# Performance work log

Hardware: AMD Instinct MI355X
Metric: run time of the kernel (lower is better)

## Reference

```python
import jax, jax.numpy as jnp
import numpy as np

D_MODEL = 1024
N_HEADS = 16
D_K = 64  # per-head dim and the scaling denominator used by the module
NEG = -1e9  # stand-in for -inf in masked_fill (rows are never fully masked)


def setup_inputs() -> dict:
    key = jax.random.key(0)
    ks = jax.random.split(key, 8)
    B, M, N = 2, 2048, 2048
    q = jax.random.normal(ks[0], (B, M, D_MODEL), dtype=jnp.float32)
    k = jax.random.normal(ks[1], (B, N, D_MODEL), dtype=jnp.float32)
    v = jax.random.normal(ks[2], (B, N, D_MODEL), dtype=jnp.float32)
    mask = jax.random.randint(ks[3], (B, M, N), 0, 2).astype(jnp.bool_)
    # xavier_uniform for square [d,d] weights: limit = sqrt(6/(d+d))
    lim = float(np.sqrt(6.0 / (D_MODEL + D_MODEL)))
    Wq = jax.random.uniform(ks[4], (D_MODEL, D_MODEL), jnp.float32, -lim, lim)
    Wk = jax.random.uniform(ks[5], (D_MODEL, D_MODEL), jnp.float32, -lim, lim)
    Wv = jax.random.uniform(ks[6], (D_MODEL, D_MODEL), jnp.float32, -lim, lim)
    Wo = jax.random.uniform(ks[7], (D_MODEL, D_MODEL), jnp.float32, -lim, lim)
    return {"q": q, "k": k, "v": v, "mask": mask,
            "Wq": Wq, "Wk": Wk, "Wv": Wv, "Wo": Wo}


def _split_heads(x):
    # (B, S, D) -> (B, H, S, Dh); the torch split/cat-on-batch trick is
    # mathematically identical to this standard head reshape.
    B, S, _ = x.shape
    return x.reshape(B, S, N_HEADS, D_K).transpose(0, 2, 1, 3)


def reference(q, k, v, mask, Wq, Wk, Wv, Wo):
    qw = _split_heads(q @ Wq.T)  # (B,H,M,Dh)
    kw = _split_heads(k @ Wk.T)  # (B,H,N,Dh)
    vw = _split_heads(v @ Wv.T)  # (B,H,N,Dh)
    scores = jnp.einsum('bhmd,bhnd->bhmn', qw, kw)
    scores = jnp.where(mask[:, None, :, :], NEG, scores)
    attn = jax.nn.softmax(scores / jnp.sqrt(jnp.float32(D_K)), axis=-1)
    ctx = jnp.einsum('bhmn,bhnd->bhmd', attn, vw)
    B, _, M, _ = ctx.shape
    ctx = ctx.transpose(0, 2, 1, 3).reshape(B, M, D_MODEL)
    return ctx @ Wo.T
```

## Files before the change

kernel.cpp:

```cpp
#include <hip/hip_runtime.h>
#include <hip/hip_bf16.h>
#include <stdint.h>
#include <string.h>

#define SEQ   2048
#define DM    1024
#define NH    16
#define NB    2

typedef __attribute__((ext_vector_type(8))) short bf16x8;
typedef __attribute__((ext_vector_type(4))) float f32x4;
typedef unsigned short u16;
typedef unsigned int   u32;

__device__ __forceinline__ u16 f2bf(float f) {
    u32 u = __float_as_uint(f);
    u += 0x7FFF + ((u >> 16) & 1);
    return (u16)(u >> 16);
}
__device__ __forceinline__ u32 pk2bf(float a, float b) {
    __hip_bfloat162 p = __float22bfloat162_rn(make_float2(a, b));
    u32 u; memcpy(&u, &p, 4); return u;
}
__device__ __forceinline__ float fexp2(float x) {
#if __has_builtin(__builtin_amdgcn_exp2f)
    return __builtin_amdgcn_exp2f(x);
#else
    return exp2f(x);
#endif
}
__device__ __forceinline__ void gl_lds16(const void* g, void* l) {
    __builtin_amdgcn_global_load_lds(
        (const __attribute__((address_space(1))) u32*)g,
        (__attribute__((address_space(3))) u32*)l, 16, 0, 0);
}

struct CvtArgs {
    const float* s[7];
    u16* d[7];
    float scale[7];
    int start[8];
};
__global__ __launch_bounds__(256) void cvt_kernel(CvtArgs a) {
    int bid = blockIdx.x;
    int seg = 0;
#pragma unroll
    for (int i = 1; i < 7; ++i) if (bid >= a.start[i]) seg = i;
    float sc = a.scale[seg];
    size_t base = (size_t)(bid - a.start[seg]) * 2048 + threadIdx.x * 8;
    const float4* s4 = (const float4*)(a.s[seg] + base);
    float4 x = s4[0], y = s4[1];
    u32 r[4];
    r[0] = pk2bf(x.x*sc, x.y*sc); r[1] = pk2bf(x.z*sc, x.w*sc);
    r[2] = pk2bf(y.x*sc, y.y*sc); r[3] = pk2bf(y.z*sc, y.w*sc);
    *(uint4*)(a.d[seg] + base) = *(uint4*)r;
}

__global__ void maskpack_kernel(const int* __restrict__ mask,
                                unsigned int* __restrict__ bits) {
    int gid = blockIdx.x * 256 + threadIdx.x;
    int m = mask[gid];
    unsigned long long bal = __ballot(m != 0);
    int lane = threadIdx.x & 63;
    if (lane == 0)       bits[gid >> 5] = (u32)(bal & 0xFFFFFFFFull);
    else if (lane == 32) bits[gid >> 5] = (u32)(bal >> 32);
}

template<int RT>
__device__ __forceinline__ void gemm_body(const u16* __restrict__ A,
                                          const u16* __restrict__ Bm,
                                          void* __restrict__ Y,
                                          int rtile, int ctile, int mode,
                                          u16* sA, u16* sB) {
    constexpr int ABUF = RT * 32 * 32;
    constexpr int BBUF = 128 * 32;
    const int tid  = threadIdx.x;
    const int wv   = tid >> 6, lane = tid & 63;
    const int quad = lane >> 4, ln = lane & 15;
    const int wr   = wv >> 1,  wc  = wv & 1;

    const int lr4 = lane >> 2;
    const int lcc = ((lane & 3) ^ ((lane >> 3) & 3)) * 8;

    const u16* gA[RT/2]; u16* lA[RT/2];
#pragma unroll
    for (int s = 0; s < RT/2; ++s) {
        int seg = wv * (RT/2) + s;
        gA[s] = A + (size_t)(rtile * (RT*32) + seg*16 + lr4) * 1024 + lcc;
        lA[s] = sA + seg * 512;
    }
    const u16* gB[2]; u16* lB[2];
#pragma unroll
    for (int s = 0; s < 2; ++s) {
        int seg = wv * 2 + s;
        gB[s] = Bm + (size_t)(ctile * 128 + seg*16 + lr4) * 1024 + lcc;
        lB[s] = sB + seg * 512;
    }

    f32x4 acc[RT][4];
#pragma unroll
    for (int i = 0; i < RT; ++i)
#pragma unroll
        for (int j = 0; j < 4; ++j) acc[i][j] = (f32x4){0.f,0.f,0.f,0.f};

    const int c0 = (quad ^ ((ln >> 1) & 3)) * 8;

#pragma unroll
    for (int s = 0; s < RT/2; ++s) gl_lds16(gA[s], lA[s]);
#pragma unroll
    for (int s = 0; s < 2; ++s)    gl_lds16(gB[s], lB[s]);

    for (int kt = 0; kt < 32; ++kt) {
        __syncthreads();
        if (kt < 31) {
            int nb = (kt + 1) & 1;
#pragma unroll
            for (int s = 0; s < RT/2; ++s)
                gl_lds16(gA[s] + (kt+1)*32, lA[s] + nb*ABUF);
#pragma unroll
            for (int s = 0; s < 2; ++s)
                gl_lds16(gB[s] + (kt+1)*32, lB[s] + nb*BBUF);
        }
        const u16* sAb = sA + (kt & 1) * ABUF;
        const u16* sBb = sB + (kt & 1) * BBUF;
        bf16x8 af[RT], bfr[4];
#pragma unroll
        for (int rt = 0; rt < RT; ++rt)
            af[rt] = *(const bf16x8*)(sAb + (wr*(RT*16) + rt*16 + ln) * 32 + c0);
#pragma unroll
        for (int ct = 0; ct < 4; ++ct)
            bfr[ct] = *(const bf16x8*)(sBb + (wc*64 + ct*16 + ln) * 32 + c0);
#pragma unroll
        for (int rt = 0; rt < RT; ++rt)
#pragma unroll
            for (int ct = 0; ct < 4; ++ct)
                acc[rt][ct] = __builtin_amdgcn_mfma_f32_16x16x32_bf16(
                    af[rt], bfr[ct], acc[rt][ct], 0, 0, 0);
    }

#pragma unroll
    for (int rt = 0; rt < RT; ++rt) {
#pragma unroll
        for (int ct = 0; ct < 4; ++ct) {
#pragma unroll
            for (int i = 0; i < 4; ++i) {
                int R = rtile*(RT*32) + wr*(RT*16) + rt*16 + quad*4 + i;
                int C = ctile*128 + wc*64 + ct*16 + ln;
                float val = acc[rt][ct][i];
                if (mode == 0) {
                    int b = R >> 11, s = R & 2047, h = C >> 6, d = C & 63;
                    ((u16*)Y)[((size_t)((b*NH + h) * SEQ + s) << 6) + d] = f2bf(val);
                } else if (mode == 1) {
                    int h = R >> 6, d = R & 63, b = C >> 11, n = C & 2047;
                    ((u16*)Y)[((size_t)((b*NH + h) * 64 + d) << 11) + n] = f2bf(val);
                } else {
                    ((float*)Y)[(size_t)R * 1024 + C] = val;
                }
            }
        }
    }
}

struct QKVArgs { const u16* A[3]; const u16* B[3]; u16* Y[3]; };

__global__ __launch_bounds__(256) void gemm_qkv(QKVArgs g) {
    __shared__ u16 sA[2 * 128 * 32];
    __shared__ u16 sB[2 * 128 * 32];
    int z = blockIdx.z;
    if (z == 2)
        gemm_body<4>(g.A[2], g.B[2], g.Y[2], blockIdx.y, blockIdx.x, 1, sA, sB);
    else
        gemm_body<4>(g.A[z], g.B[z], g.Y[z], blockIdx.x, blockIdx.y, 0, sA, sB);
}

__global__ __launch_bounds__(256) void gemm_out(const u16* __restrict__ A,
                                                const u16* __restrict__ Bm,
                                                float* __restrict__ Y) {
    __shared__ u16 sA[2 * 64 * 32];
    __shared__ u16 sB[2 * 128 * 32];
    gemm_body<2>(A, Bm, Y, blockIdx.x, blockIdx.y, 2, sA, sB);
}

__global__ __launch_bounds__(256) void attn_kernel(
    const u16* __restrict__ qw,
    const u16* __restrict__ kw,
    const u16* __restrict__ vt,
    const u32* __restrict__ mbits,
    u16* __restrict__ ctx) {

    constexpr int PST = 68;
    __shared__ u16 sK[2 * 64 * 64];
    __shared__ u16 sV[2 * 64 * 64];
    __shared__ u16 sP[4 * 32 * PST];

    const int mtile = blockIdx.x;
    const int bh    = blockIdx.y;
    const int b     = bh >> 4;
    const int tid   = threadIdx.x;
    const int wv    = tid >> 6, lane = tid & 63;
    const int quad  = lane >> 4, ln = lane & 15;
    const int m0    = mtile * 128;

    const size_t hbase = (size_t)bh * SEQ * 64;

    bf16x8 qf[2][2];
#pragma unroll
    for (int mt = 0; mt < 2; ++mt) {
        const u16* qp = qw + hbase + (size_t)(m0 + (wv*2+mt)*16 + ln) * 64 + quad*8;
        qf[mt][0] = *(const bf16x8*)(qp);
        qf[mt][1] = *(const bf16x8*)(qp + 32);
    }

    f32x4 o[2][4], lsum[2];
#pragma unroll
    for (int mt = 0; mt < 2; ++mt) {
        lsum[mt] = (f32x4){0.f,0.f,0.f,0.f};
#pragma unroll
        for (int j = 0; j < 4; ++j) o[mt][j] = (f32x4){0.f,0.f,0.f,0.f};
    }

    bf16x8 ones;
#pragma unroll
    for (int i = 0; i < 8; ++i) ones[i] = (short)0x3F80;

    const u32* mbase = mbits + (size_t)(b * SEQ + m0 + wv*32 + quad*4) * 64;
    const u32 mlo = 1u << ln;
    const u32 mhi = 1u << (ln + 16);

    const int lr = lane >> 3;
    const int lc = (lane & 7) ^ lr;
    const u16* gK[2]; const u16* gV[2];
    u16 *lK[2], *lV[2];
#pragma unroll
    for (int s = 0; s < 2; ++s) {
        int seg = s * 4 + wv;
        gK[s] = kw + hbase + (size_t)(seg*8 + lr) * 64 + lc*8;
        gV[s] = vt + hbase + (size_t)(seg*8 + lr) * SEQ + lc*8;
        lK[s] = sK + seg * 512;
        lV[s] = sV + seg * 512;
    }

    const int c0 = (quad ^ (ln & 7)) * 8;
    u16* sPw = sP + wv * 32 * PST;

#pragma unroll
    for (int s = 0; s < 2; ++s) { gl_lds16(gK[s], lK[s]); gl_lds16(gV[s], lV[s]); }
    uint2 wwA[2][4];
#pragma unroll
    for (int mt = 0; mt < 2; ++mt)
#pragma unroll
        for (int i = 0; i < 4; ++i)
            wwA[mt][i] = *(const uint2*)(mbase + (mt*16 + i)*64);

    for (int nt = 0; nt < SEQ / 64; ++nt) {
        __syncthreads();
        uint2 wwB[2][4];
        if (nt < SEQ/64 - 1) {
            int nb = (nt + 1) & 1;
#pragma unroll
            for (int s = 0; s < 2; ++s) {
                gl_lds16(gK[s] + (size_t)(nt+1) * 4096, lK[s] + nb*4096);
                gl_lds16(gV[s] + (nt+1) * 64,           lV[s] + nb*4096);
            }
#pragma unroll
            for (int mt = 0; mt < 2; ++mt)
#pragma unroll
                for (int i = 0; i < 4; ++i)
                    wwB[mt][i] = *(const uint2*)(mbase + (mt*16 + i)*64 + (nt+1)*2);
        }
        const u16* sKb = sK + (nt & 1) * 4096;
        const u16* sVb = sV + (nt & 1) * 4096;

        f32x4 s4[2][4];
#pragma unroll
        for (int ct = 0; ct < 4; ++ct) {
            const u16* kp = sKb + (ct*16 + ln) * 64;
            bf16x8 k0 = *(const bf16x8*)(kp + c0);
            bf16x8 k1 = *(const bf16x8*)(kp + (c0 ^ 32));
#pragma unroll
            for (int mt = 0; mt < 2; ++mt) {
                f32x4 z = (f32x4){0.f, 0.f, 0.f, 0.f};
                z = __builtin_amdgcn_mfma_f32_16x16x32_bf16(qf[mt][0], k0, z, 0, 0, 0);
                z = __builtin_amdgcn_mfma_f32_16x16x32_bf16(qf[mt][1], k1, z, 0, 0, 0);
                s4[mt][ct] = z;
            }
        }

#pragma unroll
        for (int mt = 0; mt < 2; ++mt) {
#pragma unroll
            for (int ct = 0; ct < 4; ++ct) {
                const u32 mb = (ct & 1) ? mhi : mlo;
#pragma unroll
                for (int ii = 0; ii < 4; ii += 2) {
                    u32 w0 = (ct & 2) ? wwA[mt][ii].y   : wwA[mt][ii].x;
                    u32 w1 = (ct & 2) ? wwA[mt][ii+1].y : wwA[mt][ii+1].x;
                    float p0 = fexp2((w0 & mb) ? -1e9f : s4[mt][ct][ii]);
                    float p1 = fexp2((w1 & mb) ? -1e9f : s4[mt][ct][ii+1]);
                    u32 u = pk2bf(p0, p1);
                    int row = mt*16 + quad*4 + ii;
                    sPw[ row    * PST + ct*16 + ln] = (u16)u;
                    sPw[(row+1) * PST + ct*16 + ln] = (u16)(u >> 16);
                }
            }
        }

        bf16x8 pf[2][2];
#pragma unroll
        for (int mt = 0; mt < 2; ++mt) {
            const u16* pp = sPw + (mt*16 + ln) * PST;
            pf[mt][0] = *(const bf16x8*)(pp + quad*8);
            pf[mt][1] = *(const bf16x8*)(pp + 32 + quad*8);
            lsum[mt] = __builtin_amdgcn_mfma_f32_16x16x32_bf16(pf[mt][0], ones, lsum[mt], 0, 0, 0);
            lsum[mt] = __builtin_amdgcn_mfma_f32_16x16x32_bf16(pf[mt][1], ones, lsum[mt], 0, 0, 0);
        }
#pragma unroll
        for (int ct = 0; ct < 4; ++ct) {
            const u16* vp = sVb + (ct*16 + ln) * 64;
            bf16x8 v0 = *(const bf16x8*)(vp + c0);
            bf16x8 v1 = *(const bf16x8*)(vp + (c0 ^ 32));
#pragma unroll
            for (int mt = 0; mt < 2; ++mt) {
                o[mt][ct] = __builtin_amdgcn_mfma_f32_16x16x32_bf16(pf[mt][0], v0, o[mt][ct], 0, 0, 0);
                o[mt][ct] = __builtin_amdgcn_mfma_f32_16x16x32_bf16(pf[mt][1], v1, o[mt][ct], 0, 0, 0);
            }
        }

#pragma unroll
        for (int mt = 0; mt < 2; ++mt)
#pragma unroll
            for (int i = 0; i < 4; ++i)
                wwA[mt][i] = wwB[mt][i];
    }

#pragma unroll
    for (int mt = 0; mt < 2; ++mt)
#pragma unroll
        for (int i = 0; i < 4; ++i) {
            float inv = 1.f / lsum[mt][i];
            int m = m0 + (wv*2+mt)*16 + quad*4 + i;
            size_t base = ((size_t)(b * SEQ + m) << 10) + (bh & 15) * 64;
#pragma unroll
            for (int ct = 0; ct < 4; ++ct)
                ctx[base + ct*16 + ln] = f2bf(o[mt][ct][i] * inv);
        }
}

extern "C" void kernel_launch(void* const* d_in, const int* in_sizes, int n_in,
                              void* d_out, int out_size, void* d_ws, size_t ws_size,
                              hipStream_t stream) {
    const float* q    = (const float*)d_in[0];
    const float* k    = (const float*)d_in[1];
    const float* v    = (const float*)d_in[2];
    const int*   mask = (const int*)d_in[3];
    const float* Wq   = (const float*)d_in[4];
    const float* Wk   = (const float*)d_in[5];
    const float* Wv   = (const float*)d_in[6];
    const float* Wo   = (const float*)d_in[7];
    float* out = (float*)d_out;

    char* ws = (char*)d_ws;
    const size_t SZH = (size_t)NB * SEQ * DM * 2;
    const size_t SZW = (size_t)DM * DM * 2;
    u16* qw   = (u16*)(ws);
    u16* kw   = (u16*)(ws + SZH);
    u16* vt   = (u16*)(ws + 2*SZH);
    u16* ctx  = (u16*)(ws + 3*SZH);
    u16* vb   = ctx;
    u32* mbits= (u32*)(ws + 4*SZH);
    u16* qb   = (u16*)(ws + 4*SZH + (1u<<20));
    u16* kb   = (u16*)(ws + 4*SZH + (1u<<20) + SZH);
    u16* Wqb  = (u16*)(ws + 4*SZH + (1u<<20) + 2*SZH);
    u16* Wkb  = (u16*)((char*)Wqb + SZW);
    u16* Wvb  = (u16*)((char*)Wqb + 2*SZW);
    u16* Wob  = (u16*)((char*)Wqb + 3*SZW);

    const float CSC = 0.18033688011112042f;

    CvtArgs ca;
    ca.s[0]=q;  ca.d[0]=qb;  ca.scale[0]=1.f;
    ca.s[1]=k;  ca.d[1]=kb;  ca.scale[1]=1.f;
    ca.s[2]=v;  ca.d[2]=vb;  ca.scale[2]=1.f;
    ca.s[3]=Wq; ca.d[3]=Wqb; ca.scale[3]=CSC;
    ca.s[4]=Wk; ca.d[4]=Wkb; ca.scale[4]=1.f;
    ca.s[5]=Wv; ca.d[5]=Wvb; ca.scale[5]=1.f;
    ca.s[6]=Wo; ca.d[6]=Wob; ca.scale[6]=1.f;
    int st[8] = {0, 2048, 4096, 6144, 6656, 7168, 7680, 8192};
    for (int i = 0; i < 8; ++i) ca.start[i] = st[i];
    cvt_kernel<<<dim3(8192), dim3(256), 0, stream>>>(ca);

    maskpack_kernel<<<dim3(NB*SEQ*SEQ/256), dim3(256), 0, stream>>>(mask, mbits);

    QKVArgs ga;
    ga.A[0]=qb;  ga.B[0]=Wqb; ga.Y[0]=qw;
    ga.A[1]=kb;  ga.B[1]=Wkb; ga.Y[1]=kw;
    ga.A[2]=Wvb; ga.B[2]=vb;  ga.Y[2]=vt;
    gemm_qkv<<<dim3(32, 8, 3), dim3(256), 0, stream>>>(ga);

    attn_kernel<<<dim3(SEQ/128, NB*NH), dim3(256), 0, stream>>>(qw, kw, vt, mbits, ctx);

    gemm_out<<<dim3(64, 8), dim3(256), 0, stream>>>(ctx, Wob, out);
}
```

Measured before the change: 296.8 us.

## Triple-buffer GEMM and attention loads with vmcnt-gated barriers and transposed score MFMA

Moves the GEMM and attention main loops from double to triple buffering with a two-tile prefetch distance. Each plain __syncthreads is replaced by an s_waitcnt on a partial vmcnt followed by s_barrier, so one tile of loads can stay in flight across the barrier. In attention, the score MFMA operands are swapped so each lane holds one row's scores, letting P be written as packed 8-byte stores and mask bits be read with one word per row. The cost is more LDS per block and fragile hand-counted vmcnt values that must match the number of loads in flight.

```diff
diff --git a/kernel.cpp b/kernel.cpp
--- a/kernel.cpp
+++ b/kernel.cpp
@@ -34,6 +34,10 @@
         (const __attribute__((address_space(1))) u32*)g,
         (__attribute__((address_space(3))) u32*)l, 16, 0, 0);
 }
+__device__ __forceinline__ void wbar_vm3() { asm volatile("s_waitcnt vmcnt(3)\ns_barrier" ::: "memory"); }
+__device__ __forceinline__ void wbar_vm4() { asm volatile("s_waitcnt vmcnt(4)\ns_barrier" ::: "memory"); }
+__device__ __forceinline__ void wbar_vm6() { asm volatile("s_waitcnt vmcnt(6)\ns_barrier" ::: "memory"); }
+__device__ __forceinline__ void vm_drain() { asm volatile("s_waitcnt vmcnt(0)" ::: "memory"); }
 
 struct CvtArgs {
     const float* s[7];
@@ -109,20 +113,22 @@
     for (int s = 0; s < RT/2; ++s) gl_lds16(gA[s], lA[s]);
 #pragma unroll
     for (int s = 0; s < 2; ++s)    gl_lds16(gB[s], lB[s]);
-
+#pragma unroll
+    for (int s = 0; s < RT/2; ++s) gl_lds16(gA[s] + 32, lA[s] + ABUF);
+#pragma unroll
+    for (int s = 0; s < 2; ++s)    gl_lds16(gB[s] + 32, lB[s] + BBUF);
+
+    int bc = 0, bp = 2;
     for (int kt = 0; kt < 32; ++kt) {
-        __syncthreads();
-        if (kt < 31) {
-            int nb = (kt + 1) & 1;
-#pragma unroll
-            for (int s = 0; s < RT/2; ++s)
-                gl_lds16(gA[s] + (kt+1)*32, lA[s] + nb*ABUF);
-#pragma unroll
-            for (int s = 0; s < 2; ++s)
-                gl_lds16(gB[s] + (kt+1)*32, lB[s] + nb*BBUF);
-        }
-        const u16* sAb = sA + (kt & 1) * ABUF;
-        const u16* sBb = sB + (kt & 1) * BBUF;
+        if (RT == 4) wbar_vm4(); else wbar_vm3();
+        int pk = (kt + 2) & 31;
+#pragma unroll
+        for (int s = 0; s < RT/2; ++s) gl_lds16(gA[s] + pk*32, lA[s] + bp*ABUF);
+#pragma unroll
+        for (int s = 0; s < 2; ++s)    gl_lds16(gB[s] + pk*32, lB[s] + bp*BBUF);
+
+        const u16* sAb = sA + bc * ABUF;
+        const u16* sBb = sB + bc * BBUF;
         bf16x8 af[RT], bfr[4];
 #pragma unroll
         for (int rt = 0; rt < RT; ++rt)
@@ -136,7 +142,11 @@
             for (int ct = 0; ct < 4; ++ct)
                 acc[rt][ct] = __builtin_amdgcn_mfma_f32_16x16x32_bf16(
                     af[rt], bfr[ct], acc[rt][ct], 0, 0, 0);
-    }
+
+        bc = (bc == 2) ? 0 : bc + 1;
+        bp = (bp == 2) ? 0 : bp + 1;
+    }
+    vm_drain();
 
 #pragma unroll
     for (int rt = 0; rt < RT; ++rt) {
@@ -164,8 +174,8 @@
 struct QKVArgs { const u16* A[3]; const u16* B[3]; u16* Y[3]; };
 
 __global__ __launch_bounds__(256) void gemm_qkv(QKVArgs g) {
-    __shared__ u16 sA[2 * 128 * 32];
-    __shared__ u16 sB[2 * 128 * 32];
+    __shared__ u16 sA[3 * 128 * 32];
+    __shared__ u16 sB[3 * 128 * 32];
     int z = blockIdx.z;
     if (z == 2)
         gemm_body<4>(g.A[2], g.B[2], g.Y[2], blockIdx.y, blockIdx.x, 1, sA, sB);
@@ -176,8 +186,8 @@
 __global__ __launch_bounds__(256) void gemm_out(const u16* __restrict__ A,
                                                 const u16* __restrict__ Bm,
                                                 float* __restrict__ Y) {
-    __shared__ u16 sA[2 * 64 * 32];
-    __shared__ u16 sB[2 * 128 * 32];
+    __shared__ u16 sA[3 * 64 * 32];
+    __shared__ u16 sB[3 * 128 * 32];
     gemm_body<2>(A, Bm, Y, blockIdx.x, blockIdx.y, 2, sA, sB);
 }
 
@@ -188,10 +198,10 @@
     const u32* __restrict__ mbits,
     u16* __restrict__ ctx) {
 
-    constexpr int PST = 68;
-    __shared__ u16 sK[2 * 64 * 64];
-    __shared__ u16 sV[2 * 64 * 64];
-    __shared__ u16 sP[4 * 32 * PST];
+    constexpr int RSD = 36;
+    __shared__ u16 sK[3 * 4096];
+    __shared__ u16 sV[3 * 4096];
+    __shared__ u32 sPd[4 * 32 * RSD];
 
     const int mtile = blockIdx.x;
     const int bh    = blockIdx.y;
@@ -206,7 +216,7 @@
     bf16x8 qf[2][2];
 #pragma unroll
     for (int mt = 0; mt < 2; ++mt) {
-        const u16* qp = qw + hbase + (size_t)(m0 + (wv*2+mt)*16 + ln) * 64 + quad*8;
+        const u16* qp = qw + hbase + (size_t)(m0 + wv*32 + mt*16 + ln) * 64 + quad*8;
         qf[mt][0] = *(const bf16x8*)(qp);
         qf[mt][1] = *(const bf16x8*)(qp + 32);
     }
@@ -223,9 +233,10 @@
 #pragma unroll
     for (int i = 0; i < 8; ++i) ones[i] = (short)0x3F80;
 
-    const u32* mbase = mbits + (size_t)(b * SEQ + m0 + wv*32 + quad*4) * 64;
-    const u32 mlo = 1u << ln;
-    const u32 mhi = 1u << (ln + 16);
+    const u32* mrow[2];
+#pragma unroll
+    for (int mt = 0; mt < 2; ++mt)
+        mrow[mt] = mbits + (size_t)(b*SEQ + m0 + wv*32 + mt*16 + ln) * 64;
 
     const int lr = lane >> 3;
     const int lc = (lane & 7) ^ lr;
@@ -241,35 +252,37 @@
     }
 
     const int c0 = (quad ^ (ln & 7)) * 8;
-    u16* sPw = sP + wv * 32 * PST;
+    u32* sPw = sPd + wv * 32 * RSD;
+    const u16* sP16 = (const u16*)sPd;
 
 #pragma unroll
     for (int s = 0; s < 2; ++s) { gl_lds16(gK[s], lK[s]); gl_lds16(gV[s], lV[s]); }
-    uint2 wwA[2][4];
-#pragma unroll
-    for (int mt = 0; mt < 2; ++mt)
-#pragma unroll
-        for (int i = 0; i < 4; ++i)
-            wwA[mt][i] = *(const uint2*)(mbase + (mt*16 + i)*64);
-
+    uint2 wwA[2], wwB[2], wwC[2];
+#pragma unroll
+    for (int mt = 0; mt < 2; ++mt) wwA[mt] = *(const uint2*)(mrow[mt]);
+#pragma unroll
+    for (int s = 0; s < 2; ++s) {
+        gl_lds16(gK[s] + 4096, lK[s] + 4096);
+        gl_lds16(gV[s] + 64,   lV[s] + 4096);
+    }
+#pragma unroll
+    for (int mt = 0; mt < 2; ++mt) wwB[mt] = *(const uint2*)(mrow[mt] + 2);
+
+    int bc = 0, bp = 2;
     for (int nt = 0; nt < SEQ / 64; ++nt) {
-        __syncthreads();
-        uint2 wwB[2][4];
-        if (nt < SEQ/64 - 1) {
-            int nb = (nt + 1) & 1;
-#pragma unroll
-            for (int s = 0; s < 2; ++s) {
-                gl_lds16(gK[s] + (size_t)(nt+1) * 4096, lK[s] + nb*4096);
-                gl_lds16(gV[s] + (nt+1) * 64,           lV[s] + nb*4096);
-            }
-#pragma unroll
-            for (int mt = 0; mt < 2; ++mt)
-#pragma unroll
-                for (int i = 0; i < 4; ++i)
-                    wwB[mt][i] = *(const uint2*)(mbase + (mt*16 + i)*64 + (nt+1)*2);
-        }
-        const u16* sKb = sK + (nt & 1) * 4096;
-        const u16* sVb = sV + (nt & 1) * 4096;
+        wbar_vm6();
+        int pidx = (nt + 2) & 31;
+#pragma unroll
+        for (int s = 0; s < 2; ++s) {
+            gl_lds16(gK[s] + (size_t)pidx * 4096, lK[s] + bp*4096);
+            gl_lds16(gV[s] + pidx * 64,           lV[s] + bp*4096);
+        }
+#pragma unroll
+        for (int mt = 0; mt < 2; ++mt)
+            wwC[mt] = *(const uint2*)(mrow[mt] + pidx*2);
+
+        const u16* sKb = sK + bc * 4096;
+        const u16* sVb = sV + bc * 4096;
 
         f32x4 s4[2][4];
 #pragma unroll
@@ -280,65 +293,62 @@
 #pragma unroll
             for (int mt = 0; mt < 2; ++mt) {
                 f32x4 z = (f32x4){0.f, 0.f, 0.f, 0.f};
-                z = __builtin_amdgcn_mfma_f32_16x16x32_bf16(qf[mt][0], k0, z, 0, 0, 0);
-                z = __builtin_amdgcn_mfma_f32_16x16x32_bf16(qf[mt][1], k1, z, 0, 0, 0);
+                z = __builtin_amdgcn_mfma_f32_16x16x32_bf16(k0, qf[mt][0], z, 0, 0, 0);
+                z = __builtin_amdgcn_mfma_f32_16x16x32_bf16(k1, qf[mt][1], z, 0, 0, 0);
                 s4[mt][ct] = z;
             }
         }
 
 #pragma unroll
         for (int mt = 0; mt < 2; ++mt) {
+            u32 w0 = wwA[mt].x >> (quad * 4);
+            u32 w1 = wwA[mt].y >> (quad * 4);
 #pragma unroll
             for (int ct = 0; ct < 4; ++ct) {
-                const u32 mb = (ct & 1) ? mhi : mlo;
-#pragma unroll
-                for (int ii = 0; ii < 4; ii += 2) {
-                    u32 w0 = (ct & 2) ? wwA[mt][ii].y   : wwA[mt][ii].x;
-                    u32 w1 = (ct & 2) ? wwA[mt][ii+1].y : wwA[mt][ii+1].x;
-                    float p0 = fexp2((w0 & mb) ? -1e9f : s4[mt][ct][ii]);
-                    float p1 = fexp2((w1 & mb) ? -1e9f : s4[mt][ct][ii+1]);
-                    u32 u = pk2bf(p0, p1);
-                    int row = mt*16 + quad*4 + ii;
-                    sPw[ row    * PST + ct*16 + ln] = (u16)u;
-                    sPw[(row+1) * PST + ct*16 + ln] = (u16)(u >> 16);
+                u32 wsel = (ct & 2) ? w1 : w0;
+                float p[4];
+#pragma unroll
+                for (int i = 0; i < 4; ++i) {
+                    bool msk = (wsel >> ((ct & 1) * 16 + i)) & 1u;
+                    p[i] = fexp2(msk ? -1e9f : s4[mt][ct][i]);
                 }
+                uint2 pk;
+                pk.x = pk2bf(p[0], p[1]);
+                pk.y = pk2bf(p[2], p[3]);
+                *(uint2*)(sPw + (mt*16 + ln) * RSD + ct*8 + quad*2) = pk;
             }
         }
 
-        bf16x8 pf[2][2];
 #pragma unroll
         for (int mt = 0; mt < 2; ++mt) {
-            const u16* pp = sPw + (mt*16 + ln) * PST;
-            pf[mt][0] = *(const bf16x8*)(pp + quad*8);
-            pf[mt][1] = *(const bf16x8*)(pp + 32 + quad*8);
-            lsum[mt] = __builtin_amdgcn_mfma_f32_16x16x32_bf16(pf[mt][0], ones, lsum[mt], 0, 0, 0);
-            lsum[mt] = __builtin_amdgcn_mfma_f32_16x16x32_bf16(pf[mt][1], ones, lsum[mt], 0, 0, 0);
-        }
-#pragma unroll
-        for (int ct = 0; ct < 4; ++ct) {
-            const u16* vp = sVb + (ct*16 + ln) * 64;
-            bf16x8 v0 = *(const bf16x8*)(vp + c0);
-            bf16x8 v1 = *(const bf16x8*)(vp + (c0 ^ 32));
-#pragma unroll
-            for (int mt = 0; mt < 2; ++mt) {
-                o[mt][ct] = __builtin_amdgcn_mfma_f32_16x16x32_bf16(pf[mt][0], v0, o[mt][ct], 0, 0, 0);
-                o[mt][ct] = __builtin_amdgcn_mfma_f32_16x16x32_bf16(pf[mt][1], v1, o[mt][ct], 0, 0, 0);
+            const u16* pp = sP16 + (wv*32 + mt*16 + ln) * 72;
+            bf16x8 pf0 = *(const bf16x8*)(pp + quad*8);
+            bf16x8 pf1 = *(const bf16x8*)(pp + 32 + quad*8);
+            lsum[mt] = __builtin_amdgcn_mfma_f32_16x16x32_bf16(pf0, ones, lsum[mt], 0, 0, 0);
+            lsum[mt] = __builtin_amdgcn_mfma_f32_16x16x32_bf16(pf1, ones, lsum[mt], 0, 0, 0);
+#pragma unroll
+            for (int ct = 0; ct < 4; ++ct) {
+                const u16* vp = sVb + (ct*16 + ln) * 64;
+                bf16x8 v0 = *(const bf16x8*)(vp + c0);
+                bf16x8 v1 = *(const bf16x8*)(vp + (c0 ^ 32));
+                o[mt][ct] = __builtin_amdgcn_mfma_f32_16x16x32_bf16(pf0, v0, o[mt][ct], 0, 0, 0);
+                o[mt][ct] = __builtin_amdgcn_mfma_f32_16x16x32_bf16(pf1, v1, o[mt][ct], 0, 0, 0);
             }
         }
 
-#pragma unroll
-        for (int mt = 0; mt < 2; ++mt)
-#pragma unroll
-            for (int i = 0; i < 4; ++i)
-                wwA[mt][i] = wwB[mt][i];
-    }
+        wwA[0] = wwB[0]; wwA[1] = wwB[1];
+        wwB[0] = wwC[0]; wwB[1] = wwC[1];
+        bc = (bc == 2) ? 0 : bc + 1;
+        bp = (bp == 2) ? 0 : bp + 1;
+    }
+    vm_drain();
 
 #pragma unroll
     for (int mt = 0; mt < 2; ++mt)
 #pragma unroll
         for (int i = 0; i < 4; ++i) {
             float inv = 1.f / lsum[mt][i];
-            int m = m0 + (wv*2+mt)*16 + quad*4 + i;
+            int m = m0 + wv*32 + mt*16 + quad*4 + i;
             size_t base = ((size_t)(b * SEQ + m) << 10) + (bh & 15) * 64;
 #pragma unroll
             for (int ct = 0; ct < 4; ++ct)
```

New measurement: 276.3 us. 1.07x faster.
